# Kernel optimization log

Hardware: AMD Instinct MI355X
Metric: run time of the kernel (lower is better)

The kernel has to match this reference:

```python
import jax, jax.numpy as jnp
import numpy as np

EPS = 1e-5
NUM_HEADS = 12

def layer_norm(x, g, b):
    mu = jnp.mean(x, axis=-1, keepdims=True)
    var = jnp.var(x, axis=-1, keepdims=True)
    return (x - mu) * jax.lax.rsqrt(var + EPS) * g + b

def setup_inputs() -> dict:
    key = jax.random.key(0)
    ks = jax.random.split(key, 8)
    B, N, Dv, Ds, F = 8, 1024, 768, 512, 768
    def w(k, shape, fan_in):
        return jax.random.normal(k, shape, jnp.float32) * (fan_in ** -0.5)
    return dict(
        visual_features=jax.random.normal(ks[0], (B, N, Dv), jnp.float32),
        semantic_features=jax.random.normal(ks[1], (B, Ds), jnp.float32),
        Wq=w(ks[2], (F, Ds), Ds),
        Wk=w(ks[3], (F, Dv), Dv),
        Wv=w(ks[4], (F, Dv), Dv),
        Wo=w(ks[5], (Dv, F), F),
        bo=jnp.zeros((Dv,), jnp.float32),
        Wg=w(ks[6], (Dv, Dv + Ds), Dv + Ds),
        bg=jnp.zeros((Dv,), jnp.float32),
        gv=jnp.ones((Dv,), jnp.float32),
        bv=jnp.zeros((Dv,), jnp.float32),
        gs=jnp.ones((Ds,), jnp.float32),
        bs=jnp.zeros((Ds,), jnp.float32),
    )

def reference(visual_features, semantic_features, Wq, Wk, Wv, Wo, bo, Wg, bg, gv, bv, gs, bs):
    B, N, Dv = visual_features.shape
    F = Wq.shape[0]
    H = NUM_HEADS
    dh = F // H
    scale = dh ** -0.5
    vis_n = layer_norm(visual_features, gv, bv)           # (B,N,Dv)
    sem_n = layer_norm(semantic_features, gs, bs)         # (B,Ds) — LN over last dim; broadcast-invariant
    # Query is identical for every patch row -> exact single-query collapse of the N x N attention
    q = (sem_n @ Wq.T).reshape(B, H, dh)                  # (B,H,dh)
    k = (vis_n @ Wk.T).reshape(B, N, H, dh).transpose(0, 2, 1, 3)  # (B,H,N,dh)
    v = (vis_n @ Wv.T).reshape(B, N, H, dh).transpose(0, 2, 1, 3)  # (B,H,N,dh)
    scores = jnp.einsum('bhd,bhnd->bhn', q, k) * scale
    attn = jax.nn.softmax(scores, axis=-1)
    ctx = jnp.einsum('bhn,bhnd->bhd', attn, v).reshape(B, F)
    attended = ctx @ Wo.T + bo                            # (B,Dv), same for all N rows (dropout in eval = identity)
    sem_b = jnp.broadcast_to(semantic_features[:, None, :], (B, N, semantic_features.shape[-1]))
    gate_in = jnp.concatenate([visual_features, sem_b], axis=-1)   # (B,N,Dv+Ds)
    gate = jax.nn.sigmoid(gate_in @ Wg.T + bg)            # (B,N,Dv)
    return visual_features + gate * attended[:, None, :]
```

## Files before the change

kernel.cpp:

```cpp
#include <hip/hip_runtime.h>
#include <hip/hip_bf16.h>
#include <math.h>


typedef __attribute__((ext_vector_type(8))) short bf16x8;
typedef __attribute__((ext_vector_type(4))) float f32x4;

#define LN_EPS 1e-5f

__device__ __forceinline__ float bf2f(__hip_bfloat16 h){ return __bfloat162float(h); }

union bfpk8 { uint4 u; __hip_bfloat16 h[8]; };
union bfpk4 { uint2 u; __hip_bfloat16 h[4]; };

__device__ __align__(16) __hip_bfloat16 c_x[8*1024*768];
__device__ __align__(16) __hip_bfloat16 c_sem[8*512];
__device__ __align__(16) __hip_bfloat16 c_Wq[768*512];
__device__ __align__(16) __hip_bfloat16 c_Wk[768*768];
__device__ __align__(16) __hip_bfloat16 c_Wv[768*768];
__device__ __align__(16) __hip_bfloat16 c_Wo[768*768];
__device__ __align__(16) __hip_bfloat16 c_bo[768];
__device__ __align__(16) __hip_bfloat16 c_Wg[768*1280];
__device__ __align__(16) __hip_bfloat16 c_bg[768];
__device__ __align__(16) __hip_bfloat16 c_gv[768];
__device__ __align__(16) __hip_bfloat16 c_bv[768];
__device__ __align__(16) __hip_bfloat16 c_gs[512];
__device__ __align__(16) __hip_bfloat16 c_bs[512];

__device__ __align__(16) __hip_bfloat16 g_gqb[8*16*768];
__device__ __align__(16) float g_A[8*12*768];
__device__ __align__(16) float g_sgq[96];
__device__ __align__(16) float g_bq[96];
__device__ __align__(16) float g_mu[8192];
__device__ __align__(16) float g_rstd[8192];
__device__ __align__(16) float g_w[8*12*1024];
__device__ __align__(16) float g_C[96];
__device__ __align__(16) float g_ctx[8*768];
__device__ __align__(16) float g_att[8*768];
__device__ __align__(16) float g_gsem[8*768];

__device__ __forceinline__ int detect_bf16(const void* gv_raw){
    return ((const unsigned int*)gv_raw)[0] == 0x3F803F80u;
}

__device__ __forceinline__ void conv8(const void* __restrict__ src,
                                      __hip_bfloat16* __restrict__ dst,
                                      int g, int isb){
    if(isb){
        ((uint4*)dst)[g] = ((const uint4*)src)[g];
    } else {
        const float* s = (const float*)src + (size_t)g*8;
        bfpk8 o;
        #pragma unroll
        for(int e=0;e<8;e++) o.h[e] = __float2bfloat16(s[e]);
        ((uint4*)dst)[g] = o.u;
    }
}

#define ING_BLKS 1925
__global__ void k_ingest(const void* s1, const void* s2, const void* s3,
                         const void* s4, const void* s5, const void* s6, const void* s7,
                         const void* s8, const void* s9, const void* s10, const void* s11,
                         const void* s12){
    int i = blockIdx.x*256 + threadIdx.x;
    int isb = detect_bf16(s9);
    if     (i <    512) conv8(s1, c_sem, i,         isb);
    else if(i <  49664) conv8(s2, c_Wq,  i-   512,  isb);
    else if(i < 123392) conv8(s3, c_Wk,  i- 49664,  isb);
    else if(i < 197120) conv8(s4, c_Wv,  i-123392,  isb);
    else if(i < 270848) conv8(s5, c_Wo,  i-197120,  isb);
    else if(i < 270944) conv8(s6, c_bo,  i-270848,  isb);
    else if(i < 393824) conv8(s7, c_Wg,  i-270944,  isb);
    else if(i < 393920) conv8(s8, c_bg,  i-393824,  isb);
    else if(i < 394016) conv8(s9, c_gv,  i-393920,  isb);
    else if(i < 394112) conv8(s10,c_bv,  i-394016,  isb);
    else if(i < 394176) conv8(s11,c_gs,  i-394112,  isb);
    else if(i < 394240) conv8(s12,c_bs,  i-394176,  isb);
    else if(i < 467968) g_A[i-394240]   = 0.f;
    else if(i < 468064) g_sgq[i-467968] = 0.f;
    else if(i < 468160) g_bq[i-468064]  = 0.f;
    else if(i < 474304) g_ctx[i-468160] = 0.f;
    else if(i < 480448) g_att[i-474304] = 0.f;
    else if(i < 492736){
        uint4 z; z.x=0; z.y=0; z.z=0; z.w=0;
        ((uint4*)g_gqb)[i-480448] = z;
    }
}

__global__ __launch_bounds__(256)
void k_pre(){
    __shared__ __align__(16) unsigned char smem[33536];
    const int t = threadIdx.x;
    const int id = blockIdx.x;
    if(id < 144){
        float* s_semn = (float*)smem;
        float* s_q2   = (float*)(smem + 16384);
        __hip_bfloat16* s_wk = (__hip_bfloat16*)(smem + 18432);
        const int h = id / 12;
        const int c0 = (id % 12)*64;
        {
            int b = t>>5, l = t&31;
            bfpk8 p0, p1;
            p0.u = *(const uint4*)(c_sem + b*512 + l*16);
            p1.u = *(const uint4*)(c_sem + b*512 + l*16 + 8);
            float v[16], s = 0.f, s2 = 0.f;
            #pragma unroll
            for(int e=0;e<8;e++){ v[e]   = bf2f(p0.h[e]); s += v[e];   s2 += v[e]*v[e]; }
            #pragma unroll
            for(int e=0;e<8;e++){ v[8+e] = bf2f(p1.h[e]); s += v[8+e]; s2 += v[8+e]*v[8+e]; }
            #pragma unroll
            for(int o=16;o>0;o>>=1){ s += __shfl_xor(s,o); s2 += __shfl_xor(s2,o); }
            float mu = s*(1.f/512.f);
            float rstd = rsqrtf(s2*(1.f/512.f) - mu*mu + LN_EPS);
            bfpk8 g0, g1, b0, b1;
            g0.u = *(const uint4*)(c_gs + l*16);   g1.u = *(const uint4*)(c_gs + l*16 + 8);
            b0.u = *(const uint4*)(c_bs + l*16);   b1.u = *(const uint4*)(c_bs + l*16 + 8);
            #pragma unroll
            for(int e=0;e<8;e++){
                s_semn[b*512 + l*16 + e]     = (v[e]-mu)*rstd*bf2f(g0.h[e]) + bf2f(b0.h[e]);
                s_semn[b*512 + l*16 + 8 + e] = (v[8+e]-mu)*rstd*bf2f(g1.h[e]) + bf2f(b1.h[e]);
            }
        }
        for(int i=t;i<512;i+=256){
            int j = i>>3, sl = i&7;
            *(uint4*)(s_wk + j*64 + sl*8) = *(const uint4*)(c_Wk + (size_t)(h*64+j)*768 + c0 + sl*8);
        }
        __syncthreads();
        {
            int fi = t & 63, bp = t >> 6;
            int f = h*64 + fi;
            const __hip_bfloat16* wr = c_Wq + (size_t)f*512;
            float a0 = 0.f, a1 = 0.f;
            for(int i0=0;i0<512;i0+=8){
                bfpk8 pk; pk.u = *(const uint4*)(wr + i0);
                #pragma unroll
                for(int c=0;c<8;c++){
                    float wv = bf2f(pk.h[c]);
                    a0 += wv*s_semn[bp*512 + i0 + c];
                    a1 += wv*s_semn[(bp+4)*512 + i0 + c];
                }
            }
            s_q2[bp*64+fi] = a0; s_q2[(bp+4)*64+fi] = a1;
        }
        __syncthreads();
        const int dvl = t & 63, w = t >> 6;
        const int dv = c0 + dvl;
        float a0 = 0.f, a1 = 0.f;
        #pragma unroll 8
        for(int j=0;j<64;j++){
            float wk = bf2f(s_wk[j*64+dvl]);
            a0 += s_q2[w*64+j]*wk;
            a1 += s_q2[(w+4)*64+j]*wk;
        }
        float gvv = bf2f(c_gv[dv]), bvv = bf2f(c_bv[dv]);
        {
            float g = a0*gvv;
            g_gqb[((size_t)w*16+h)*768 + dv] = __float2bfloat16(g);
            float sg = g, sb = bvv*a0;
            #pragma unroll
            for(int o=32;o>0;o>>=1){ sg += __shfl_xor(sg,o); sb += __shfl_xor(sb,o); }
            if(dvl==0){ atomicAdd(&g_sgq[w*12+h], sg); atomicAdd(&g_bq[w*12+h], sb); }
        }
        {
            float g = a1*gvv;
            g_gqb[((size_t)(w+4)*16+h)*768 + dv] = __float2bfloat16(g);
            float sg = g, sb = bvv*a1;
            #pragma unroll
            for(int o=32;o>0;o>>=1){ sg += __shfl_xor(sg,o); sb += __shfl_xor(sb,o); }
            if(dvl==0){ atomicAdd(&g_sgq[(w+4)*12+h], sg); atomicAdd(&g_bq[(w+4)*12+h], sb); }
        }
    } else {
        float* s_sem = (float*)smem;
        __hip_bfloat16* s_wg = (__hip_bfloat16*)(smem + 16384);
        float* s_part = (float*)(smem + 33024);
        const int col0 = (id - 144)*16;
        for(int i=t;i<512;i+=256){
            bfpk8 p; p.u = *(const uint4*)(c_sem + i*8);
            #pragma unroll
            for(int e=0;e<8;e++) s_sem[i*8+e] = bf2f(p.h[e]);
        }
        for(int i=t;i<16*64;i+=256){
            int rl = i>>6, c = i&63;
            *(uint4*)(s_wg + rl*520 + c*8) =
                *(const uint4*)(c_Wg + (size_t)(col0+rl)*1280 + 768 + c*8);
        }
        __syncthreads();
        const int cl = t&15, bh = t>>4, bb = bh&7, half = bh>>3;
        const __hip_bfloat16* wr = s_wg + cl*520 + half*256;
        const float* sr = s_sem + bb*512 + half*256;
        float a = 0.f;
        for(int k=0;k<256;k+=8){
            bfpk8 p; p.u = *(const uint4*)(wr + k);
            #pragma unroll
            for(int e=0;e<8;e++) a += bf2f(p.h[e])*sr[k+e];
        }
        if(half) s_part[t&127] = a;
        __syncthreads();
        if(!half) g_gsem[bb*768 + col0 + cl] = a + s_part[t&127];
    }
}

__global__ __launch_bounds__(256)
void k_scores(const void* __restrict__ xraw, const void* __restrict__ gvraw){
    __shared__ float s_acc[256*4];
    __shared__ float s_s[4][16], s_s2[4][16];
    __shared__ float s_mu[16], s_rstd[16];
    const int b = blockIdx.y;
    const int t = threadIdx.x, lane = t & 63, w = t >> 6;
    const int isb = detect_bf16(gvraw);
    const int fr = lane & 15, quad = lane >> 4;
    const int n_tile = blockIdx.x*16;
    const size_t row = (size_t)b*1024 + n_tile + fr;
    const __hip_bfloat16* Bp = g_gqb + (size_t)b*16*768 + (size_t)fr*768;
    const int k0 = w*192;

    f32x4 acc = {};
    float s = 0.f, s2 = 0.f;
    if(isb){
        const __hip_bfloat16* xr = (const __hip_bfloat16*)xraw + row*768;
        for(int kb=k0; kb<k0+192; kb+=32){
            bfpk8 pk; pk.u = *(const uint4*)(xr + kb + quad*8);
            *(uint4*)(c_x + row*768 + kb + quad*8) = pk.u;
            #pragma unroll
            for(int e=0;e<8;e++){ float f = bf2f(pk.h[e]); s += f; s2 += f*f; }
            bf16x8 bfrag = *(const bf16x8*)(Bp + kb + quad*8);
            acc = __builtin_amdgcn_mfma_f32_16x16x32_bf16(*(const bf16x8*)&pk, bfrag, acc, 0,0,0);
        }
    } else {
        const float* xr = (const float*)xraw + row*768;
        for(int kb=k0; kb<k0+192; kb+=32){
            f32x4 x0 = *(const f32x4*)(xr + kb + quad*8);
            f32x4 x1 = *(const f32x4*)(xr + kb + quad*8 + 4);
            bfpk8 pk;
            #pragma unroll
            for(int e=0;e<4;e++){ pk.h[e]   = __float2bfloat16(x0[e]); s += x0[e]; s2 += x0[e]*x0[e]; }
            #pragma unroll
            for(int e=0;e<4;e++){ pk.h[4+e] = __float2bfloat16(x1[e]); s += x1[e]; s2 += x1[e]*x1[e]; }
            *(uint4*)(c_x + row*768 + kb + quad*8) = pk.u;
            bf16x8 bfrag = *(const bf16x8*)(Bp + kb + quad*8);
            acc = __builtin_amdgcn_mfma_f32_16x16x32_bf16(*(const bf16x8*)&pk, bfrag, acc, 0,0,0);
        }
    }
    s  += __shfl_xor(s, 16);  s  += __shfl_xor(s, 32);
    s2 += __shfl_xor(s2, 16); s2 += __shfl_xor(s2, 32);
    *(f32x4*)&s_acc[t*4] = acc;
    if(quad == 0){ s_s[w][fr] = s; s_s2[w][fr] = s2; }
    __syncthreads();
    if(w == 0){
        #pragma unroll
        for(int ww=1;ww<4;ww++){
            f32x4 o = *(const f32x4*)&s_acc[(ww*64+lane)*4];
            acc[0]+=o[0]; acc[1]+=o[1]; acc[2]+=o[2]; acc[3]+=o[3];
        }
        if(quad == 0){
            float st  = s_s[0][fr]+s_s[1][fr]+s_s[2][fr]+s_s[3][fr];
            float st2 = s_s2[0][fr]+s_s2[1][fr]+s_s2[2][fr]+s_s2[3][fr];
            float mu = st*(1.f/768.f);
            float rstd = rsqrtf(st2*(1.f/768.f) - mu*mu + LN_EPS);
            g_mu[b*1024 + n_tile + fr] = mu;
            g_rstd[b*1024 + n_tile + fr] = rstd;
            s_mu[fr] = mu; s_rstd[fr] = rstd;
        }
    }
    __syncthreads();
    if(w == 0 && fr < 12){
        float sgqh = g_sgq[b*12+fr];
        float bqh  = g_bq [b*12+fr];
        #pragma unroll
        for(int r=0;r<4;r++){
            int rr = quad*4 + r;
            float val = 0.125f*( s_rstd[rr]*(acc[r] - s_mu[rr]*sgqh) + bqh );
            g_w[((size_t)b*12+fr)*1024 + n_tile + rr] = val;
        }
    }
}

__global__ void k_softmax(){
    int bh = blockIdx.x, b = bh/12, t = threadIdx.x;
    float* sc = g_w + (size_t)bh*1024;
    f32x4 v = *(f32x4*)(sc + t*4);
    float m = fmaxf(fmaxf(v[0],v[1]), fmaxf(v[2],v[3]));
    __shared__ float redm[4], reds[4], redc[4];
    #pragma unroll
    for(int o=32;o>0;o>>=1) m = fmaxf(m, __shfl_xor(m,o));
    if((t&63)==0) redm[t>>6] = m;
    __syncthreads();
    m = fmaxf(fmaxf(redm[0],redm[1]), fmaxf(redm[2],redm[3]));
    float e0=expf(v[0]-m), e1=expf(v[1]-m), e2=expf(v[2]-m), e3=expf(v[3]-m);
    float s = e0+e1+e2+e3;
    #pragma unroll
    for(int o=32;o>0;o>>=1) s += __shfl_xor(s,o);
    if((t&63)==0) reds[t>>6] = s;
    __syncthreads();
    s = reds[0]+reds[1]+reds[2]+reds[3];
    float inv = 1.f/s;
    f32x4 rv = *(f32x4*)(g_rstd + b*1024 + t*4);
    f32x4 mv = *(f32x4*)(g_mu   + b*1024 + t*4);
    f32x4 o4;
    o4[0]=e0*inv*rv[0]; o4[1]=e1*inv*rv[1]; o4[2]=e2*inv*rv[2]; o4[3]=e3*inv*rv[3];
    *(f32x4*)(sc + t*4) = o4;
    float cp = o4[0]*mv[0] + o4[1]*mv[1] + o4[2]*mv[2] + o4[3]*mv[3];
    #pragma unroll
    for(int o=32;o>0;o>>=1) cp += __shfl_xor(cp,o);
    if((t&63)==0) redc[t>>6] = cp;
    __syncthreads();
    if(t==0) g_C[bh] = redc[0]+redc[1]+redc[2]+redc[3];
}

__global__ void k_accA(){
    __shared__ float s_w[12*128];
    int t = threadIdx.x, b = blockIdx.z, n0 = blockIdx.y*128;
    for(int i=t;i<12*128;i+=256){
        int h = i>>7, n = i&127;
        s_w[i] = g_w[((size_t)b*12+h)*1024 + n0 + n];
    }
    __syncthreads();
    int dv = blockIdx.x*256 + t;
    float acc[12] = {0,0,0,0,0,0,0,0,0,0,0,0};
    for(int n=0;n<128;n++){
        float xv = bf2f(c_x[(size_t)(b*1024+n0+n)*768 + dv]);
        #pragma unroll
        for(int h=0;h<12;h++) acc[h] += s_w[h*128+n]*xv;
    }
    #pragma unroll
    for(int h=0;h<12;h++) atomicAdd(&g_A[((size_t)b*12+h)*768 + dv], acc[h]);
}

__global__ void k_ctx(){
    __shared__ float s_wvis[8*68];
    int h = blockIdx.x, ch = blockIdx.y, t = threadIdx.x;
    int base = ch*64;
    {
        int b = t>>6, dvl = t&63;
        int dv = base + dvl;
        s_wvis[b*68+dvl] = bf2f(c_gv[dv])*(g_A[((size_t)b*12+h)*768+dv] - g_C[b*12+h]) + bf2f(c_bv[dv]);
    }
    __syncthreads();
    int f = h*64 + (t>>3), b = t&7;
    const __hip_bfloat16* wr = c_Wv + (size_t)f*768 + base;
    float acc = 0.f;
    #pragma unroll
    for(int d0=0;d0<64;d0+=8){
        bfpk8 pk; pk.u = *(const uint4*)(wr + d0);
        #pragma unroll
        for(int c=0;c<8;c++) acc += s_wvis[b*68 + d0 + c]*bf2f(pk.h[c]);
    }
    atomicAdd(&g_ctx[b*768+f], acc);
}

__global__ void k_att(){
    __shared__ float s_ctx[8*68];
    int ch = blockIdx.y, t = threadIdx.x;
    int base = ch*64;
    {
        int b = t>>6, fl = t&63;
        s_ctx[b*68+fl] = g_ctx[b*768 + base + fl];
    }
    __syncthreads();
    int dv2 = blockIdx.x*64 + (t>>3), b = t&7;
    const __hip_bfloat16* wr = c_Wo + (size_t)dv2*768 + base;
    float acc = (ch==0) ? bf2f(c_bo[dv2]) : 0.f;
    #pragma unroll
    for(int f0=0;f0<64;f0+=8){
        bfpk8 pk; pk.u = *(const uint4*)(wr + f0);
        #pragma unroll
        for(int c=0;c<8;c++) acc += s_ctx[b*68 + f0 + c]*bf2f(pk.h[c]);
    }
    atomicAdd(&g_att[b*768+dv2], acc);
}

__device__ __forceinline__ void stage_gate(int buf, int kb, int m0, int n0,
                                           __hip_bfloat16* As, __hip_bfloat16* Bs,
                                           int wave, int lane){
    const int rl = lane >> 2;
    const int kc = ((lane & 3) ^ ((rl >> 1) & 3))*8;
    #pragma unroll
    for(int s=0;s<2;s++){
        int c = wave + 4*s;
        int row = c*16 + rl;
        const __hip_bfloat16* gp = c_x + (size_t)(m0+row)*768 + kb + kc;
        __builtin_amdgcn_global_load_lds(
            (const __attribute__((address_space(1))) void*)gp,
            (__attribute__((address_space(3))) void*)(As + buf*4096 + c*512),
            16, 0, 0);
    }
    {
        int c = wave;
        int row = c*16 + rl;
        const __hip_bfloat16* gp = c_Wg + (size_t)(n0+row)*1280 + kb + kc;
        __builtin_amdgcn_global_load_lds(
            (const __attribute__((address_space(1))) void*)gp,
            (__attribute__((address_space(3))) void*)(Bs + buf*2048 + c*512),
            16, 0, 0);
    }
}

__global__ __launch_bounds__(256)
void k_gate(void* __restrict__ outv, const void* __restrict__ gv_raw){
    __shared__ __align__(16) __hip_bfloat16 As[3*128*32];
    __shared__ __align__(16) __hip_bfloat16 Bs[3*64*32];
    const int isb = detect_bf16(gv_raw);
    const int t = threadIdx.x;
    const int lin  = blockIdx.y*12 + blockIdx.x;
    const int wgid = (lin & 7)*96 + (lin >> 3);
    const int n0 = (wgid % 12)*64;
    const int m0 = (wgid / 12)*128;
    const int b_blk = m0 >> 10;
    const int lane = t & 63, wave = t >> 6;
    const int wm = (wave>>1)*64, wn = (wave&1)*32;
    const int fr = lane & 15, quad = lane >> 4;
    const int sq = (quad ^ ((fr >> 1) & 3))*8;

    f32x4 acc[4][2] = {};

    stage_gate(0,  0, m0, n0, As, Bs, wave, lane);
    stage_gate(1, 32, m0, n0, As, Bs, wave, lane);
    #pragma unroll
    for(int it=0; it<24; ++it){
        if(it < 23) asm volatile("s_waitcnt vmcnt(3)" ::: "memory");
        else        asm volatile("s_waitcnt vmcnt(0)" ::: "memory");
        asm volatile("s_waitcnt lgkmcnt(0)" ::: "memory");
        asm volatile("s_barrier" ::: "memory");
        const __hip_bfloat16* Ab = As + (it%3)*4096;
        const __hip_bfloat16* Bb = Bs + (it%3)*2048;
        bf16x8 af[4], bfr[2];
        #pragma unroll
        for(int i=0;i<4;i++) af[i]  = *(const bf16x8*)(Ab + (wm + i*16 + fr)*32 + sq);
        #pragma unroll
        for(int j=0;j<2;j++) bfr[j] = *(const bf16x8*)(Bb + (wn + j*16 + fr)*32 + sq);
        #pragma unroll
        for(int i=0;i<4;i++)
            #pragma unroll
            for(int j=0;j<2;j++)
                acc[i][j] = __builtin_amdgcn_mfma_f32_16x16x32_bf16(af[i], bfr[j], acc[i][j], 0,0,0);
        if(it < 22)
            stage_gate((it+2)%3, (it+2)*32, m0, n0, As, Bs, wave, lane);
    }

    #pragma unroll
    for(int j=0;j<2;j++){
        int col = n0 + wn + j*16 + fr;
        float attv = g_att[b_blk*768 + col];
        float bgv  = bf2f(c_bg[col]) + g_gsem[b_blk*768 + col];
        #pragma unroll
        for(int i=0;i<4;i++){
            int mbase = m0 + wm + i*16 + quad*4;
            #pragma unroll
            for(int r=0;r<4;r++){
                int m = mbase + r;
                float g = acc[i][j][r] + bgv;
                g = fminf(fmaxf(g, -60.f), 60.f);
                float gate = 1.f/(1.f + expf(-g));
                float xv = bf2f(c_x[(size_t)m*768 + col]);
                float val = xv + gate*attv;
                size_t idx = (size_t)m*768 + col;
                if(isb) ((__hip_bfloat16*)outv)[idx] = __float2bfloat16(val);
                else    ((float*)outv)[idx] = val;
            }
        }
    }
}

extern "C" void kernel_launch(void* const* d_in, const int* in_sizes, int n_in,
                              void* d_out, int out_size, void* d_ws, size_t ws_size,
                              hipStream_t stream){
    (void)in_sizes; (void)n_in; (void)out_size; (void)d_ws; (void)ws_size;

    k_ingest<<<dim3(ING_BLKS), dim3(256), 0, stream>>>(d_in[1], d_in[2], d_in[3],
                                                       d_in[4], d_in[5], d_in[6], d_in[7],
                                                       d_in[8], d_in[9], d_in[10], d_in[11],
                                                       d_in[12]);
    k_pre<<<dim3(192), dim3(256), 0, stream>>>();
    k_scores<<<dim3(64,8), dim3(256), 0, stream>>>(d_in[0], d_in[9]);
    k_softmax<<<dim3(96), dim3(256), 0, stream>>>();
    k_accA<<<dim3(3,8,8), dim3(256), 0, stream>>>();
    k_ctx<<<dim3(12,12), dim3(512), 0, stream>>>();
    k_att<<<dim3(12,12), dim3(512), 0, stream>>>();
    k_gate<<<dim3(12,64), dim3(256), 0, stream>>>(d_out, d_in[9]);
}
```

Before: 196.3 us.

## Fuse ingest into precompute kernel and fold softmax into accumulation kernel

Merges the weight conversion/zeroing kernel with the precompute kernel, which now reads Wq, Wk, sem, gs and bs directly from the raw inputs instead of converted copies. The softmax kernel is removed: each accA block recomputes per-head max and sum over 1024 scores and applies the exp-normalise-rstd scaling while staging weights. Atomic accumulation of sgq/bq is replaced by per-chunk partial writes summed later, which drops the zeroing dependency. This removes two launches and several global round trips, at the cost of redundant softmax reductions in every accA block.

```diff
diff --git a/kernel.cpp b/kernel.cpp
--- a/kernel.cpp
+++ b/kernel.cpp
@@ -11,12 +11,8 @@
 __device__ __forceinline__ float bf2f(__hip_bfloat16 h){ return __bfloat162float(h); }
 
 union bfpk8 { uint4 u; __hip_bfloat16 h[8]; };
-union bfpk4 { uint2 u; __hip_bfloat16 h[4]; };
 
 __device__ __align__(16) __hip_bfloat16 c_x[8*1024*768];
-__device__ __align__(16) __hip_bfloat16 c_sem[8*512];
-__device__ __align__(16) __hip_bfloat16 c_Wq[768*512];
-__device__ __align__(16) __hip_bfloat16 c_Wk[768*768];
 __device__ __align__(16) __hip_bfloat16 c_Wv[768*768];
 __device__ __align__(16) __hip_bfloat16 c_Wo[768*768];
 __device__ __align__(16) __hip_bfloat16 c_bo[768];
@@ -24,13 +20,11 @@
 __device__ __align__(16) __hip_bfloat16 c_bg[768];
 __device__ __align__(16) __hip_bfloat16 c_gv[768];
 __device__ __align__(16) __hip_bfloat16 c_bv[768];
-__device__ __align__(16) __hip_bfloat16 c_gs[512];
-__device__ __align__(16) __hip_bfloat16 c_bs[512];
 
 __device__ __align__(16) __hip_bfloat16 g_gqb[8*16*768];
 __device__ __align__(16) float g_A[8*12*768];
-__device__ __align__(16) float g_sgq[96];
-__device__ __align__(16) float g_bq[96];
+__device__ __align__(16) float g_sgqp[12*96];
+__device__ __align__(16) float g_bqp[12*96];
 __device__ __align__(16) float g_mu[8192];
 __device__ __align__(16) float g_rstd[8192];
 __device__ __align__(16) float g_w[8*12*1024];
@@ -57,87 +51,96 @@
     }
 }
 
-#define ING_BLKS 1925
-__global__ void k_ingest(const void* s1, const void* s2, const void* s3,
-                         const void* s4, const void* s5, const void* s6, const void* s7,
-                         const void* s8, const void* s9, const void* s10, const void* s11,
-                         const void* s12){
-    int i = blockIdx.x*256 + threadIdx.x;
-    int isb = detect_bf16(s9);
-    if     (i <    512) conv8(s1, c_sem, i,         isb);
-    else if(i <  49664) conv8(s2, c_Wq,  i-   512,  isb);
-    else if(i < 123392) conv8(s3, c_Wk,  i- 49664,  isb);
-    else if(i < 197120) conv8(s4, c_Wv,  i-123392,  isb);
-    else if(i < 270848) conv8(s5, c_Wo,  i-197120,  isb);
-    else if(i < 270944) conv8(s6, c_bo,  i-270848,  isb);
-    else if(i < 393824) conv8(s7, c_Wg,  i-270944,  isb);
-    else if(i < 393920) conv8(s8, c_bg,  i-393824,  isb);
-    else if(i < 394016) conv8(s9, c_gv,  i-393920,  isb);
-    else if(i < 394112) conv8(s10,c_bv,  i-394016,  isb);
-    else if(i < 394176) conv8(s11,c_gs,  i-394112,  isb);
-    else if(i < 394240) conv8(s12,c_bs,  i-394176,  isb);
-    else if(i < 467968) g_A[i-394240]   = 0.f;
-    else if(i < 468064) g_sgq[i-467968] = 0.f;
-    else if(i < 468160) g_bq[i-468064]  = 0.f;
-    else if(i < 474304) g_ctx[i-468160] = 0.f;
-    else if(i < 480448) g_att[i-474304] = 0.f;
-    else if(i < 492736){
-        uint4 z; z.x=0; z.y=0; z.z=0; z.w=0;
-        ((uint4*)g_gqb)[i-480448] = z;
-    }
-}
-
+__device__ __forceinline__ void load8f(const void* __restrict__ src, size_t off,
+                                       int isb, float* v){
+    if(isb){
+        bfpk8 p; p.u = *(const uint4*)((const __hip_bfloat16*)src + off);
+        #pragma unroll
+        for(int e=0;e<8;e++) v[e] = bf2f(p.h[e]);
+    } else {
+        f32x4 a = *(const f32x4*)((const float*)src + off);
+        f32x4 b = *(const f32x4*)((const float*)src + off + 4);
+        #pragma unroll
+        for(int e=0;e<4;e++){ v[e] = a[e]; v[4+e] = b[e]; }
+    }
+}
+__device__ __forceinline__ float ld1(const void* __restrict__ p, int i, int isb){
+    return isb ? bf2f(((const __hip_bfloat16*)p)[i]) : ((const float*)p)[i];
+}
+
+#define CONV_BLKS 1406
 __global__ __launch_bounds__(256)
-void k_pre(){
-    __shared__ __align__(16) unsigned char smem[33536];
+void k_ing_pre(const void* sem, const void* wq, const void* wk,
+               const void* wv, const void* wo, const void* bo_, const void* wg,
+               const void* bg_, const void* gv_, const void* bv_, const void* gs_,
+               const void* bs_){
+    __shared__ __align__(16) unsigned char smem[34816];
     const int t = threadIdx.x;
-    const int id = blockIdx.x;
+    const int isb = detect_bf16(gv_);
+    if(blockIdx.x < CONV_BLKS){
+        int i = blockIdx.x*256 + t;
+        if     (i <  73728) conv8(wv,  c_Wv, i,        isb);
+        else if(i < 147456) conv8(wo,  c_Wo, i- 73728, isb);
+        else if(i < 270336) conv8(wg,  c_Wg, i-147456, isb);
+        else if(i < 270432) conv8(bo_, c_bo, i-270336, isb);
+        else if(i < 270528) conv8(bg_, c_bg, i-270432, isb);
+        else if(i < 270624) conv8(gv_, c_gv, i-270528, isb);
+        else if(i < 270720) conv8(bv_, c_bv, i-270624, isb);
+        else if(i < 344448) g_A[i-270720]   = 0.f;
+        else if(i < 350592) g_ctx[i-344448] = 0.f;
+        else if(i < 356736) g_att[i-350592] = 0.f;
+        else if(i < 359808){
+            int j = i - 356736, b = j/384, r = j%384;
+            uint4 z; z.x=0; z.y=0; z.z=0; z.w=0;
+            ((uint4*)g_gqb)[b*1536 + 1152 + r] = z;
+        }
+        return;
+    }
+    const int id = blockIdx.x - CONV_BLKS;
     if(id < 144){
         float* s_semn = (float*)smem;
         float* s_q2   = (float*)(smem + 16384);
-        __hip_bfloat16* s_wk = (__hip_bfloat16*)(smem + 18432);
-        const int h = id / 12;
-        const int c0 = (id % 12)*64;
+        float* s_wk   = (float*)(smem + 18432);
+        const int h = id/12, c0 = (id%12)*64, cidx = id%12;
         {
             int b = t>>5, l = t&31;
-            bfpk8 p0, p1;
-            p0.u = *(const uint4*)(c_sem + b*512 + l*16);
-            p1.u = *(const uint4*)(c_sem + b*512 + l*16 + 8);
-            float v[16], s = 0.f, s2 = 0.f;
-            #pragma unroll
-            for(int e=0;e<8;e++){ v[e]   = bf2f(p0.h[e]); s += v[e];   s2 += v[e]*v[e]; }
-            #pragma unroll
-            for(int e=0;e<8;e++){ v[8+e] = bf2f(p1.h[e]); s += v[8+e]; s2 += v[8+e]*v[8+e]; }
+            float v[16];
+            load8f(sem, (size_t)b*512 + l*16,     isb, v);
+            load8f(sem, (size_t)b*512 + l*16 + 8, isb, v+8);
+            float s = 0.f, s2 = 0.f;
+            #pragma unroll
+            for(int e=0;e<16;e++){ s += v[e]; s2 += v[e]*v[e]; }
             #pragma unroll
             for(int o=16;o>0;o>>=1){ s += __shfl_xor(s,o); s2 += __shfl_xor(s2,o); }
             float mu = s*(1.f/512.f);
             float rstd = rsqrtf(s2*(1.f/512.f) - mu*mu + LN_EPS);
-            bfpk8 g0, g1, b0, b1;
-            g0.u = *(const uint4*)(c_gs + l*16);   g1.u = *(const uint4*)(c_gs + l*16 + 8);
-            b0.u = *(const uint4*)(c_bs + l*16);   b1.u = *(const uint4*)(c_bs + l*16 + 8);
-            #pragma unroll
-            for(int e=0;e<8;e++){
-                s_semn[b*512 + l*16 + e]     = (v[e]-mu)*rstd*bf2f(g0.h[e]) + bf2f(b0.h[e]);
-                s_semn[b*512 + l*16 + 8 + e] = (v[8+e]-mu)*rstd*bf2f(g1.h[e]) + bf2f(b1.h[e]);
-            }
-        }
-        for(int i=t;i<512;i+=256){
-            int j = i>>3, sl = i&7;
-            *(uint4*)(s_wk + j*64 + sl*8) = *(const uint4*)(c_Wk + (size_t)(h*64+j)*768 + c0 + sl*8);
+            float gsv[16], bsv[16];
+            load8f(gs_, l*16,     isb, gsv);  load8f(gs_, l*16 + 8, isb, gsv+8);
+            load8f(bs_, l*16,     isb, bsv);  load8f(bs_, l*16 + 8, isb, bsv+8);
+            #pragma unroll
+            for(int e=0;e<16;e++)
+                s_semn[b*512 + l*16 + e] = (v[e]-mu)*rstd*gsv[e] + bsv[e];
+        }
+        {
+            int j = t>>2, sl = t&3;
+            float wkv[16];
+            size_t off = (size_t)(h*64+j)*768 + c0 + sl*16;
+            load8f(wk, off,     isb, wkv);
+            load8f(wk, off + 8, isb, wkv+8);
+            #pragma unroll
+            for(int e=0;e<16;e++) s_wk[j*64 + sl*16 + e] = wkv[e];
         }
         __syncthreads();
         {
             int fi = t & 63, bp = t >> 6;
             int f = h*64 + fi;
-            const __hip_bfloat16* wr = c_Wq + (size_t)f*512;
             float a0 = 0.f, a1 = 0.f;
             for(int i0=0;i0<512;i0+=8){
-                bfpk8 pk; pk.u = *(const uint4*)(wr + i0);
+                float wvv[8]; load8f(wq, (size_t)f*512 + i0, isb, wvv);
                 #pragma unroll
                 for(int c=0;c<8;c++){
-                    float wv = bf2f(pk.h[c]);
-                    a0 += wv*s_semn[bp*512 + i0 + c];
-                    a1 += wv*s_semn[(bp+4)*512 + i0 + c];
+                    a0 += wvv[c]*s_semn[bp*512 + i0 + c];
+                    a1 += wvv[c]*s_semn[(bp+4)*512 + i0 + c];
                 }
             }
             s_q2[bp*64+fi] = a0; s_q2[(bp+4)*64+fi] = a1;
@@ -148,18 +151,18 @@
         float a0 = 0.f, a1 = 0.f;
         #pragma unroll 8
         for(int j=0;j<64;j++){
-            float wk = bf2f(s_wk[j*64+dvl]);
-            a0 += s_q2[w*64+j]*wk;
-            a1 += s_q2[(w+4)*64+j]*wk;
-        }
-        float gvv = bf2f(c_gv[dv]), bvv = bf2f(c_bv[dv]);
+            float wkf = s_wk[j*64+dvl];
+            a0 += s_q2[w*64+j]*wkf;
+            a1 += s_q2[(w+4)*64+j]*wkf;
+        }
+        float gvv = ld1(gv_, dv, isb), bvv = ld1(bv_, dv, isb);
         {
             float g = a0*gvv;
             g_gqb[((size_t)w*16+h)*768 + dv] = __float2bfloat16(g);
             float sg = g, sb = bvv*a0;
             #pragma unroll
             for(int o=32;o>0;o>>=1){ sg += __shfl_xor(sg,o); sb += __shfl_xor(sb,o); }
-            if(dvl==0){ atomicAdd(&g_sgq[w*12+h], sg); atomicAdd(&g_bq[w*12+h], sb); }
+            if(dvl==0){ g_sgqp[cidx*96 + w*12+h] = sg; g_bqp[cidx*96 + w*12+h] = sb; }
         }
         {
             float g = a1*gvv;
@@ -167,22 +170,32 @@
             float sg = g, sb = bvv*a1;
             #pragma unroll
             for(int o=32;o>0;o>>=1){ sg += __shfl_xor(sg,o); sb += __shfl_xor(sb,o); }
-            if(dvl==0){ atomicAdd(&g_sgq[(w+4)*12+h], sg); atomicAdd(&g_bq[(w+4)*12+h], sb); }
+            if(dvl==0){ g_sgqp[cidx*96 + (w+4)*12+h] = sg; g_bqp[cidx*96 + (w+4)*12+h] = sb; }
         }
     } else {
         float* s_sem = (float*)smem;
         __hip_bfloat16* s_wg = (__hip_bfloat16*)(smem + 16384);
         float* s_part = (float*)(smem + 33024);
         const int col0 = (id - 144)*16;
-        for(int i=t;i<512;i+=256){
-            bfpk8 p; p.u = *(const uint4*)(c_sem + i*8);
-            #pragma unroll
-            for(int e=0;e<8;e++) s_sem[i*8+e] = bf2f(p.h[e]);
+        {
+            float sv[16];
+            load8f(sem, (size_t)t*16,     isb, sv);
+            load8f(sem, (size_t)t*16 + 8, isb, sv+8);
+            #pragma unroll
+            for(int e=0;e<16;e++) s_sem[t*16+e] = sv[e];
         }
         for(int i=t;i<16*64;i+=256){
             int rl = i>>6, c = i&63;
-            *(uint4*)(s_wg + rl*520 + c*8) =
-                *(const uint4*)(c_Wg + (size_t)(col0+rl)*1280 + 768 + c*8);
+            size_t off = (size_t)(col0+rl)*1280 + 768 + c*8;
+            if(isb){
+                *(uint4*)(s_wg + rl*520 + c*8) = *(const uint4*)((const __hip_bfloat16*)wg + off);
+            } else {
+                float vv[8]; load8f(wg, off, 0, vv);
+                bfpk8 o8;
+                #pragma unroll
+                for(int e=0;e<8;e++) o8.h[e] = __float2bfloat16(vv[e]);
+                *(uint4*)(s_wg + rl*520 + c*8) = o8.u;
+            }
         }
         __syncthreads();
         const int cl = t&15, bh = t>>4, bb = bh&7, half = bh>>3;
@@ -264,8 +277,12 @@
     }
     __syncthreads();
     if(w == 0 && fr < 12){
-        float sgqh = g_sgq[b*12+fr];
-        float bqh  = g_bq [b*12+fr];
+        float sgqh = 0.f, bqh = 0.f;
+        #pragma unroll
+        for(int c=0;c<12;c++){
+            sgqh += g_sgqp[c*96 + b*12+fr];
+            bqh  += g_bqp [c*96 + b*12+fr];
+        }
         #pragma unroll
         for(int r=0;r<4;r++){
             int rr = quad*4 + r;
@@ -275,44 +292,52 @@
     }
 }
 
-__global__ void k_softmax(){
-    int bh = blockIdx.x, b = bh/12, t = threadIdx.x;
-    float* sc = g_w + (size_t)bh*1024;
-    f32x4 v = *(f32x4*)(sc + t*4);
-    float m = fmaxf(fmaxf(v[0],v[1]), fmaxf(v[2],v[3]));
-    __shared__ float redm[4], reds[4], redc[4];
-    #pragma unroll
-    for(int o=32;o>0;o>>=1) m = fmaxf(m, __shfl_xor(m,o));
-    if((t&63)==0) redm[t>>6] = m;
+__global__ __launch_bounds__(256)
+void k_accA(){
+    __shared__ float s_w[12*128];
+    __shared__ float s_m[12], s_inv[12];
+    const int t = threadIdx.x, lane = t & 63, w = t >> 6;
+    const int b = blockIdx.z, n0 = blockIdx.y*128;
+    f32x4 rv[4], mv[4];
+    #pragma unroll
+    for(int q=0;q<4;q++){
+        rv[q] = *(const f32x4*)(g_rstd + b*1024 + lane*16 + q*4);
+        mv[q] = *(const f32x4*)(g_mu   + b*1024 + lane*16 + q*4);
+    }
+    #pragma unroll
+    for(int hh=0;hh<3;hh++){
+        int h = w*3 + hh;
+        const float* sc = g_w + ((size_t)b*12+h)*1024 + lane*16;
+        f32x4 v[4];
+        #pragma unroll
+        for(int q=0;q<4;q++) v[q] = *(const f32x4*)(sc + q*4);
+        float m = -1e30f;
+        #pragma unroll
+        for(int q=0;q<4;q++)
+            #pragma unroll
+            for(int e=0;e<4;e++) m = fmaxf(m, v[q][e]);
+        #pragma unroll
+        for(int o=32;o>0;o>>=1) m = fmaxf(m, __shfl_xor(m,o));
+        float S = 0.f, P = 0.f;
+        #pragma unroll
+        for(int q=0;q<4;q++)
+            #pragma unroll
+            for(int e=0;e<4;e++){
+                float ex = expf(v[q][e]-m);
+                S += ex; P += ex*rv[q][e]*mv[q][e];
+            }
+        #pragma unroll
+        for(int o=32;o>0;o>>=1){ S += __shfl_xor(S,o); P += __shfl_xor(P,o); }
+        if(lane==0){
+            s_m[h] = m; s_inv[h] = 1.f/S;
+            if(blockIdx.x==0 && blockIdx.y==0) g_C[b*12+h] = P/S;
+        }
+    }
     __syncthreads();
-    m = fmaxf(fmaxf(redm[0],redm[1]), fmaxf(redm[2],redm[3]));
-    float e0=expf(v[0]-m), e1=expf(v[1]-m), e2=expf(v[2]-m), e3=expf(v[3]-m);
-    float s = e0+e1+e2+e3;
-    #pragma unroll
-    for(int o=32;o>0;o>>=1) s += __shfl_xor(s,o);
-    if((t&63)==0) reds[t>>6] = s;
-    __syncthreads();
-    s = reds[0]+reds[1]+reds[2]+reds[3];
-    float inv = 1.f/s;
-    f32x4 rv = *(f32x4*)(g_rstd + b*1024 + t*4);
-    f32x4 mv = *(f32x4*)(g_mu   + b*1024 + t*4);
-    f32x4 o4;
-    o4[0]=e0*inv*rv[0]; o4[1]=e1*inv*rv[1]; o4[2]=e2*inv*rv[2]; o4[3]=e3*inv*rv[3];
-    *(f32x4*)(sc + t*4) = o4;
-    float cp = o4[0]*mv[0] + o4[1]*mv[1] + o4[2]*mv[2] + o4[3]*mv[3];
-    #pragma unroll
-    for(int o=32;o>0;o>>=1) cp += __shfl_xor(cp,o);
-    if((t&63)==0) redc[t>>6] = cp;
-    __syncthreads();
-    if(t==0) g_C[bh] = redc[0]+redc[1]+redc[2]+redc[3];
-}
-
-__global__ void k_accA(){
-    __shared__ float s_w[12*128];
-    int t = threadIdx.x, b = blockIdx.z, n0 = blockIdx.y*128;
     for(int i=t;i<12*128;i+=256){
-        int h = i>>7, n = i&127;
-        s_w[i] = g_w[((size_t)b*12+h)*1024 + n0 + n];
+        int h = i>>7, n = n0 + (i&127);
+        float sc = g_w[((size_t)b*12+h)*1024 + n];
+        s_w[i] = expf(sc - s_m[h])*s_inv[h]*g_rstd[b*1024+n];
     }
     __syncthreads();
     int dv = blockIdx.x*256 + t;
@@ -466,13 +491,10 @@
                               hipStream_t stream){
     (void)in_sizes; (void)n_in; (void)out_size; (void)d_ws; (void)ws_size;
 
-    k_ingest<<<dim3(ING_BLKS), dim3(256), 0, stream>>>(d_in[1], d_in[2], d_in[3],
-                                                       d_in[4], d_in[5], d_in[6], d_in[7],
-                                                       d_in[8], d_in[9], d_in[10], d_in[11],
-                                                       d_in[12]);
-    k_pre<<<dim3(192), dim3(256), 0, stream>>>();
+    k_ing_pre<<<dim3(CONV_BLKS + 192), dim3(256), 0, stream>>>(
+        d_in[1], d_in[2], d_in[3], d_in[4], d_in[5], d_in[6], d_in[7],
+        d_in[8], d_in[9], d_in[10], d_in[11], d_in[12]);
     k_scores<<<dim3(64,8), dim3(256), 0, stream>>>(d_in[0], d_in[9]);
-    k_softmax<<<dim3(96), dim3(256), 0, stream>>>();
     k_accA<<<dim3(3,8,8), dim3(256), 0, stream>>>();
     k_ctx<<<dim3(12,12), dim3(512), 0, stream>>>();
     k_att<<<dim3(12,12), dim3(512), 0, stream>>>();
```

Result: slower. 215.2 us (+9.6%).
